# Kernel tuning notes

Measured on AMD Instinct MI355X. Metric: run time of the kernel, lower is better.

## Reference

```python
import jax, jax.numpy as jnp
import numpy as np

V_SIZE = 128000  # vocab size (v_size init arg)


def setup_inputs() -> dict:
    key = jax.random.key(0)
    k1, k2 = jax.random.split(key)
    # per-position scores -> weighting_scheme (softmax over seq dim)
    w_es = jax.random.normal(k1, (256, 2048), dtype=jnp.float32)
    # instance['x']: token ids in [0, v_size)
    x = jax.random.randint(k2, (256, 2048), 0, V_SIZE, dtype=jnp.int64)
    return {"w_es": w_es, "x": x}


def reference(w_es, x):
    # weighting_scheme(indices, w_es, instance): softmax over sequence positions
    weights = jax.nn.softmax(w_es, axis=-1)          # [B, S]
    B, S = weights.shape
    rows = jnp.arange(B)[:, None]                    # [B, 1] broadcast against [B, S]
    # scatter: w_a[b, x[b, i]] = weights[b, i]  (vectorized index_put)
    w_a = jnp.zeros((B, V_SIZE), dtype=weights.dtype).at[rows, x].set(weights)
    return (w_a, weights)
```

## Files before the change

### kernel.cpp

```cpp
#include <hip/hip_runtime.h>

#define BATCH 256
#define SEQ   2048
#define VOCAB 128000
#define HASH  4096

__global__ __launch_bounds__(256)
void softmax_scatter_kernel(const float* __restrict__ w_es,
                            const int*   __restrict__ x,
                            float* __restrict__ w_a,
                            float* __restrict__ w_out)
{
    __shared__ int   key [HASH];
    __shared__ int   maxi[HASH];
    __shared__ float red[8];

    const int r = blockIdx.x;
    const int t = threadIdx.x;
    const int lane = t & 63;
    const int wid  = t >> 6;

    for (int j = t; j < HASH; j += 256) { key[j] = -1; maxi[j] = -1; }

    const float* rowp = w_es + (size_t)r * SEQ;
    const float4 a0 = ((const float4*)rowp)[t];
    const float4 a1 = ((const float4*)rowp)[256 + t];

    float m = fmaxf(fmaxf(fmaxf(a0.x, a0.y), fmaxf(a0.z, a0.w)),
                    fmaxf(fmaxf(a1.x, a1.y), fmaxf(a1.z, a1.w)));
    #pragma unroll
    for (int off = 32; off > 0; off >>= 1)
        m = fmaxf(m, __shfl_down(m, off, 64));
    if (lane == 0) red[wid] = m;
    __syncthreads();
    m = fmaxf(fmaxf(red[0], red[1]), fmaxf(red[2], red[3]));

    float e[8];
    e[0] = __expf(a0.x - m); e[1] = __expf(a0.y - m);
    e[2] = __expf(a0.z - m); e[3] = __expf(a0.w - m);
    e[4] = __expf(a1.x - m); e[5] = __expf(a1.y - m);
    e[6] = __expf(a1.z - m); e[7] = __expf(a1.w - m);
    float s = e[0] + e[1] + e[2] + e[3] + e[4] + e[5] + e[6] + e[7];
    #pragma unroll
    for (int off = 32; off > 0; off >>= 1)
        s += __shfl_down(s, off, 64);
    if (lane == 0) red[4 + wid] = s;
    __syncthreads();
    s = red[4] + red[5] + red[6] + red[7];

    const float inv = 1.0f / s;
    float w[8];
    #pragma unroll
    for (int k = 0; k < 8; ++k) w[k] = e[k] * inv;

    float* wrow = w_out + (size_t)r * SEQ;
    ((float4*)wrow)[t]       = make_float4(w[0], w[1], w[2], w[3]);
    ((float4*)wrow)[256 + t] = make_float4(w[4], w[5], w[6], w[7]);

    const int* xrow = x + (size_t)r * SEQ;
    const int4 x0 = ((const int4*)xrow)[t];
    const int4 x1 = ((const int4*)xrow)[256 + t];
    int tok[8] = { x0.x, x0.y, x0.z, x0.w, x1.x, x1.y, x1.z, x1.w };
    int idx[8];
    #pragma unroll
    for (int k = 0; k < 4; ++k) { idx[k] = 4 * t + k; idx[4 + k] = 1024 + 4 * t + k; }

    int slot[8];
    #pragma unroll
    for (int k = 0; k < 8; ++k) {
        unsigned h = (((unsigned)tok[k] * 2654435761u) >> 16) & (HASH - 1);
        int sl = (int)h;
        while (true) {
            int prev = atomicCAS(&key[sl], -1, tok[k]);
            if (prev == -1 || prev == tok[k]) break;
            sl = (sl + 1) & (HASH - 1);
        }
        slot[k] = sl;
        atomicMax(&maxi[sl], idx[k]);
    }
    __syncthreads();

    float* warow = w_a + (size_t)r * VOCAB;
    #pragma unroll
    for (int k = 0; k < 8; ++k) {
        if (maxi[slot[k]] == idx[k])
            warow[tok[k]] = w[k];
    }
}

extern "C" void kernel_launch(void* const* d_in, const int* in_sizes, int n_in,
                              void* d_out, int out_size, void* d_ws, size_t ws_size,
                              hipStream_t stream) {
    const float* w_es = (const float*)d_in[0];
    const int*   x    = (const int*)d_in[1];

    float* out  = (float*)d_out;
    float* w_a  = out;
    float* w    = out + (size_t)BATCH * VOCAB;

    hipMemsetAsync(w_a, 0, (size_t)BATCH * VOCAB * sizeof(float), stream);

    softmax_scatter_kernel<<<BATCH, 256, 0, stream>>>(w_es, x, w_a, w);
}
```

Before: 143.1 us.

## Fuse zero-fill into scatter kernel via LDS chunked staging and nontemporal stores

Drops the separate memset of the 128 MB output. Each block now builds its row of w_a in 16K-float LDS chunks: it zeroes the chunk, scatters the winning weights into it, then writes the chunk to global memory with vectorized nontemporal stores. This removes a second pass over the large output and the random global scatter writes. In exchange each block uses about 96KB of LDS and runs only 256 blocks with one block per row, so the streaming write depends on low occupancy, and every chunk costs three barriers.

```diff
diff --git a/kernel.cpp b/kernel.cpp
--- a/kernel.cpp
+++ b/kernel.cpp
@@ -4,15 +4,20 @@
 #define SEQ   2048
 #define VOCAB 128000
 #define HASH  4096
+#define CHUNK 16384
+
+typedef float v4f __attribute__((ext_vector_type(4)));
+typedef int   v4i __attribute__((ext_vector_type(4)));
 
 __global__ __launch_bounds__(256)
-void softmax_scatter_kernel(const float* __restrict__ w_es,
-                            const int*   __restrict__ x,
-                            float* __restrict__ w_a,
-                            float* __restrict__ w_out)
+void softmax_scatter_fused(const float* __restrict__ w_es,
+                           const int*   __restrict__ x,
+                           float* __restrict__ w_a,
+                           float* __restrict__ w_out)
 {
     __shared__ int   key [HASH];
     __shared__ int   maxi[HASH];
+    __shared__ float val [CHUNK];
     __shared__ float red[8];
 
     const int r = blockIdx.x;
@@ -23,8 +28,8 @@
     for (int j = t; j < HASH; j += 256) { key[j] = -1; maxi[j] = -1; }
 
     const float* rowp = w_es + (size_t)r * SEQ;
-    const float4 a0 = ((const float4*)rowp)[t];
-    const float4 a1 = ((const float4*)rowp)[256 + t];
+    const v4f a0 = ((const v4f*)rowp)[t];
+    const v4f a1 = ((const v4f*)rowp)[256 + t];
 
     float m = fmaxf(fmaxf(fmaxf(a0.x, a0.y), fmaxf(a0.z, a0.w)),
                     fmaxf(fmaxf(a1.x, a1.y), fmaxf(a1.z, a1.w)));
@@ -54,12 +59,14 @@
     for (int k = 0; k < 8; ++k) w[k] = e[k] * inv;
 
     float* wrow = w_out + (size_t)r * SEQ;
-    ((float4*)wrow)[t]       = make_float4(w[0], w[1], w[2], w[3]);
-    ((float4*)wrow)[256 + t] = make_float4(w[4], w[5], w[6], w[7]);
+    v4f w0; w0.x = w[0]; w0.y = w[1]; w0.z = w[2]; w0.w = w[3];
+    v4f w1; w1.x = w[4]; w1.y = w[5]; w1.z = w[6]; w1.w = w[7];
+    ((v4f*)wrow)[t]       = w0;
+    ((v4f*)wrow)[256 + t] = w1;
 
     const int* xrow = x + (size_t)r * SEQ;
-    const int4 x0 = ((const int4*)xrow)[t];
-    const int4 x1 = ((const int4*)xrow)[256 + t];
+    const v4i x0 = ((const v4i*)xrow)[t];
+    const v4i x1 = ((const v4i*)xrow)[256 + t];
     int tok[8] = { x0.x, x0.y, x0.z, x0.w, x1.x, x1.y, x1.z, x1.w };
     int idx[8];
     #pragma unroll
@@ -80,11 +87,35 @@
     }
     __syncthreads();
 
+    bool win[8];
+    #pragma unroll
+    for (int k = 0; k < 8; ++k) win[k] = (maxi[slot[k]] == idx[k]);
+
     float* warow = w_a + (size_t)r * VOCAB;
-    #pragma unroll
-    for (int k = 0; k < 8; ++k) {
-        if (maxi[slot[k]] == idx[k])
-            warow[tok[k]] = w[k];
+    const v4f z4 = (v4f)0.0f;
+
+    for (int base = 0; base < VOCAB; base += CHUNK) {
+        const int cnt  = (VOCAB - base < CHUNK) ? (VOCAB - base) : CHUNK;
+        const int cnt4 = cnt >> 2;
+
+        for (int j = t; j < cnt4; j += 256)
+            ((v4f*)val)[j] = z4;
+        __syncthreads();
+
+        #pragma unroll
+        for (int k = 0; k < 8; ++k) {
+            int v = tok[k] - base;
+            if (win[k] && (unsigned)v < (unsigned)cnt)
+                val[v] = w[k];
+        }
+        __syncthreads();
+
+        float* gp = warow + base;
+        for (int j = t; j < cnt4; j += 256) {
+            v4f v4 = ((const v4f*)val)[j];
+            __builtin_nontemporal_store(v4, (v4f*)(gp + 4 * j));
+        }
+        __syncthreads();
     }
 }
 
@@ -98,7 +129,5 @@
     float* w_a  = out;
     float* w    = out + (size_t)BATCH * VOCAB;
 
-    hipMemsetAsync(w_a, 0, (size_t)BATCH * VOCAB * sizeof(float), stream);
-
-    softmax_scatter_kernel<<<BATCH, 256, 0, stream>>>(w_es, x, w_a, w);
+    softmax_scatter_fused<<<BATCH, 256, 0, stream>>>(w_es, x, w_a, w);
 }
```

Result: slower. 148.6 us (+3.9%).
